# Kernel optimization log

Hardware: AMD Instinct MI355X
Metric: run time of the kernel (lower is better)

The kernel has to match this reference:

```python
import jax, jax.numpy as jnp
import numpy as np

START_INDEX = 3
STOP_INDEX = 4
NEG = -10000.0


def _lstm_dir(x, w_ih, w_hh, b_ih, b_hh, reverse):
    """Single-direction LSTM over [T, D] with batch=1, zero init state (torch default)."""
    H = w_hh.shape[1]
    xg = x @ w_ih.T + (b_ih + b_hh)  # [T, 4H] precomputed input contribution
    def step(carry, xg_t):
        h, c = carry
        g = xg_t + h @ w_hh.T          # [4H], torch gate order i,f,g,o
        i, f, gg, o = jnp.split(g, 4)
        c = jax.nn.sigmoid(f) * c + jax.nn.sigmoid(i) * jnp.tanh(gg)
        h = jax.nn.sigmoid(o) * jnp.tanh(c)
        return (h, c), h
    init = (jnp.zeros((H,), x.dtype), jnp.zeros((H,), x.dtype))
    _, hs = jax.lax.scan(step, init, xg, reverse=reverse)
    return hs  # [T, H], time-aligned for both directions


def _viterbi(feats, transitions):
    """Vectorized log-domain Viterbi DP; transitions[next, prev]."""
    L = transitions.shape[0]
    init = jnp.full((L,), NEG, feats.dtype).at[START_INDEX].set(0.0)
    def step(fv, feat):
        scores = fv[None, :] + transitions  # [L_next, L_prev]
        fv_new = jnp.max(scores, axis=1) + feat
        return fv_new, jnp.argmax(scores, axis=1)
    fv, bps = jax.lax.scan(step, init, feats)
    terminal = fv + transitions[STOP_INDEX]
    best = jnp.argmax(terminal)
    score = terminal[best]
    def back(lbl, bp):
        return bp[lbl], lbl
    _, path = jax.lax.scan(back, best, bps, reverse=True)  # path[t] = best label at t
    return score, path


def setup_inputs() -> dict:
    E, H, L, T = 512, 1024, 5, 8192
    key = jax.random.key(0)
    ks = jax.random.split(key, 24)
    s = 1.0 / np.sqrt(H)
    u = lambda k, shape: jax.random.uniform(k, shape, jnp.float32, -s, s)
    inp = {
        "hours": jax.random.normal(ks[0], (T, E), jnp.float32),
        # layer 0 forward / reverse
        "w_ih_l0": u(ks[1], (4 * H, E)), "w_hh_l0": u(ks[2], (4 * H, H)),
        "b_ih_l0": u(ks[3], (4 * H,)), "b_hh_l0": u(ks[4], (4 * H,)),
        "w_ih_l0r": u(ks[5], (4 * H, E)), "w_hh_l0r": u(ks[6], (4 * H, H)),
        "b_ih_l0r": u(ks[7], (4 * H,)), "b_hh_l0r": u(ks[8], (4 * H,)),
        # layer 1 forward / reverse (input is 2H)
        "w_ih_l1": u(ks[9], (4 * H, 2 * H)), "w_hh_l1": u(ks[10], (4 * H, H)),
        "b_ih_l1": u(ks[11], (4 * H,)), "b_hh_l1": u(ks[12], (4 * H,)),
        "w_ih_l1r": u(ks[13], (4 * H, 2 * H)), "w_hh_l1r": u(ks[14], (4 * H, H)),
        "b_ih_l1r": u(ks[15], (4 * H,)), "b_hh_l1r": u(ks[16], (4 * H,)),
        # hidden2label
        "w_out": u(ks[17], (L, 2 * H)), "b_out": u(ks[18], (L,)),
    }
    trans = jax.random.normal(ks[19], (L, L), jnp.float32)
    trans = trans.at[START_INDEX, :].set(NEG).at[:, STOP_INDEX].set(NEG)
    inp["transitions"] = trans
    return inp


def reference(hours, w_ih_l0, w_hh_l0, b_ih_l0, b_hh_l0,
              w_ih_l0r, w_hh_l0r, b_ih_l0r, b_hh_l0r,
              w_ih_l1, w_hh_l1, b_ih_l1, b_hh_l1,
              w_ih_l1r, w_hh_l1r, b_ih_l1r, b_hh_l1r,
              w_out, b_out, transitions):
    # layer 0 bidirectional
    h0f = _lstm_dir(hours, w_ih_l0, w_hh_l0, b_ih_l0, b_hh_l0, reverse=False)
    h0b = _lstm_dir(hours, w_ih_l0r, w_hh_l0r, b_ih_l0r, b_hh_l0r, reverse=True)
    h0 = jnp.concatenate([h0f, h0b], axis=-1)  # [T, 2H]
    # layer 1 bidirectional
    h1f = _lstm_dir(h0, w_ih_l1, w_hh_l1, b_ih_l1, b_hh_l1, reverse=False)
    h1b = _lstm_dir(h0, w_ih_l1r, w_hh_l1r, b_ih_l1r, b_hh_l1r, reverse=True)
    h1 = jnp.concatenate([h1f, h1b], axis=-1)  # [T, 2H]
    feats = h1 @ w_out.T + b_out               # [T, L]
    score, path = _viterbi(feats, transitions)
    return score, path
```

## Files before the change

kernel.cpp:

```cpp
#include <hip/hip_runtime.h>
#include <hip/hip_bf16.h>
#include <stdint.h>

#define T_SEQ 8192
#define E_IN  512
#define H_DIM 1024
#define FH    4096
#define H2    2048
#define NLAB  5
#define NEGV  (-10000.0f)

typedef __attribute__((ext_vector_type(8))) short bf16x8;
typedef __attribute__((ext_vector_type(4))) float f32x4;

__device__ __forceinline__ uint32_t f2bf(float f) {
  uint32_t x = __float_as_uint(f);
  return (x + 0x7FFFu + ((x >> 16) & 1u)) >> 16;
}
__device__ __forceinline__ uint32_t pack2bf(float lo, float hi) {
  return f2bf(lo) | (f2bf(hi) << 16);
}
__device__ __forceinline__ float bf2f(uint32_t b) {
  return __uint_as_float(b << 16);
}
__device__ __forceinline__ float fsig(float x) { return 1.0f / (1.0f + __expf(-x)); }
__device__ __forceinline__ float ftanh(float x) {
  float ax = fabsf(x);
  float e = __expf(-2.0f * ax);
  float t = (1.0f - e) / (1.0f + e);
  return copysignf(t, x);
}

__global__ void bias_kernel(const float* bi0, const float* bh0,
                            const float* bi0r, const float* bh0r,
                            const float* bi1, const float* bh1,
                            const float* bi1r, const float* bh1r,
                            float* bsum) {
  int i = blockIdx.x * blockDim.x + threadIdx.x;
  int d = i >> 12, j = i & 4095;
  const float *a, *b;
  switch (d) {
    case 0:  a = bi0;  b = bh0;  break;
    case 1:  a = bi0r; b = bh0r; break;
    case 2:  a = bi1;  b = bh1;  break;
    default: a = bi1r; b = bh1r; break;
  }
  bsum[i] = a[j] + b[j];
}

template <bool AF32>
__global__ __launch_bounds__(256) void gemm_xg(const void* Aptr, const float* Bt,
                                               const float* bias, uint16_t* C, int K) {
  const int m0 = blockIdx.x * 128;
  const int n0 = blockIdx.y * 128;
  __shared__ uint32_t As[128 * 20];
  __shared__ uint32_t Bs[128 * 20];
  const int tid  = threadIdx.x;
  const int lane = tid & 63;
  const int wave = tid >> 6;
  const int wr = wave >> 1, wc = wave & 1;
  const int row = tid >> 1;
  const int seg = tid & 1;

  f32x4 acc[4][4];
#pragma unroll
  for (int i = 0; i < 4; ++i)
#pragma unroll
    for (int j = 0; j < 4; ++j)
      acc[i][j] = (f32x4){0.0f, 0.0f, 0.0f, 0.0f};

  const int nk = K / 32;
  for (int kk = 0; kk < nk; ++kk) {
    const int k0 = kk * 32;
    uint32_t* dst = &As[row * 20 + seg * 8];
    if (AF32) {
      const float4* src = (const float4*)((const float*)Aptr + (size_t)(m0 + row) * K + k0 + seg * 16);
      uint32_t w[8];
#pragma unroll
      for (int u = 0; u < 4; ++u) {
        float4 v = src[u];
        w[2 * u]     = pack2bf(v.x, v.y);
        w[2 * u + 1] = pack2bf(v.z, v.w);
      }
      ((uint4*)dst)[0] = make_uint4(w[0], w[1], w[2], w[3]);
      ((uint4*)dst)[1] = make_uint4(w[4], w[5], w[6], w[7]);
    } else {
      const uint4* src = (const uint4*)((const uint16_t*)Aptr + (size_t)(m0 + row) * K + k0 + seg * 16);
      ((uint4*)dst)[0] = src[0];
      ((uint4*)dst)[1] = src[1];
    }
    {
      const float4* src = (const float4*)(Bt + (size_t)(n0 + row) * K + k0 + seg * 16);
      uint32_t w[8];
#pragma unroll
      for (int u = 0; u < 4; ++u) {
        float4 v = src[u];
        w[2 * u]     = pack2bf(v.x, v.y);
        w[2 * u + 1] = pack2bf(v.z, v.w);
      }
      uint32_t* dstb = &Bs[row * 20 + seg * 8];
      ((uint4*)dstb)[0] = make_uint4(w[0], w[1], w[2], w[3]);
      ((uint4*)dstb)[1] = make_uint4(w[4], w[5], w[6], w[7]);
    }
    __syncthreads();

    const int mfrag = lane & 15, kq = lane >> 4;
    bf16x8 af[4], bfr[4];
#pragma unroll
    for (int i = 0; i < 4; ++i) {
      af[i]  = *(const bf16x8*)&As[(wr * 64 + i * 16 + mfrag) * 20 + kq * 4];
      bfr[i] = *(const bf16x8*)&Bs[(wc * 64 + i * 16 + mfrag) * 20 + kq * 4];
    }
#pragma unroll
    for (int i = 0; i < 4; ++i)
#pragma unroll
      for (int j = 0; j < 4; ++j)
        acc[i][j] = __builtin_amdgcn_mfma_f32_16x16x32_bf16(af[i], bfr[j], acc[i][j], 0, 0, 0);
    __syncthreads();
  }

  const int colq = lane & 15, rowq = lane >> 4;
#pragma unroll
  for (int j = 0; j < 4; ++j) {
    const int col = n0 + wc * 64 + j * 16 + colq;
    const float bv = bias[col];
    const int pcol = ((col & 1023) >> 4) * 64 + (col >> 10) * 16 + (col & 15);
#pragma unroll
    for (int i = 0; i < 4; ++i) {
#pragma unroll
      for (int r = 0; r < 4; ++r) {
        const int rrow = m0 + wr * 64 + i * 16 + rowq * 4 + r;
        C[(size_t)rrow * FH + pcol] = (uint16_t)f2bf(acc[i][j][r] + bv);
      }
    }
  }
}

__global__ __launch_bounds__(512, 2) void lstm_layer(
    const float* __restrict__ whh_f, const float* __restrict__ whh_b,
    const uint16_t* __restrict__ xg_f, const uint16_t* __restrict__ xg_b,
    uint32_t* hpub_f, uint32_t* hpub_b, uint16_t* __restrict__ hseq) {
  const int bid = blockIdx.x;
  const int dir = bid & 1;
  const int g   = bid >> 1;
  const int hb  = g * 16;
  const int tid = threadIdx.x;
  const int jj  = tid & 15;
  const int kc  = tid >> 4;
  const int lane = tid & 63;
  const int wv   = tid >> 6;

  const float*    whh  = dir ? whh_b : whh_f;
  const uint16_t* xg   = dir ? xg_b : xg_f;
  uint32_t*       hpub = dir ? hpub_b : hpub_f;
  const int colbase    = dir ? H_DIM : 0;

  __shared__ __align__(16) float h_lds[H_DIM];
  __shared__ __align__(16) float part2[8][16][4];

  float Wr[4][32];
#pragma unroll
  for (int q = 0; q < 4; ++q) {
    const float4* wrow = (const float4*)(whh + (size_t)(q * H_DIM + hb + jj) * H_DIM + kc * 32);
#pragma unroll
    for (int i4 = 0; i4 < 8; ++i4) {
      float4 v = wrow[i4];
      Wr[q][i4 * 4 + 0] = v.x; Wr[q][i4 * 4 + 1] = v.y;
      Wr[q][i4 * 4 + 2] = v.z; Wr[q][i4 * 4 + 3] = v.w;
    }
  }

  float cstate = 0.0f;

  for (int s = 0; s < T_SEQ; ++s) {
    const int t = dir ? (T_SEQ - 1 - s) : s;

    float xgv = 0.0f;
    if (tid < 64) xgv = bf2f(xg[(size_t)t * FH + g * 64 + tid]);

    if (s == 0) {
      ((float2*)h_lds)[tid] = make_float2(0.f, 0.f);
    } else {
      const uint64_t etag = ((uint64_t)(uint32_t)((s - 1) << 16) << 32) |
                            (uint32_t)((s - 1) << 16);
      unsigned long long* hp =
          (unsigned long long*)(hpub + (((s - 1) & 1) ? H_DIM : 0)) + tid;
      unsigned long long v;
      for (;;) {
        v = __hip_atomic_load(hp, __ATOMIC_RELAXED, __HIP_MEMORY_SCOPE_AGENT);
        if ((((unsigned long long)v ^ etag) & 0xFFFF0000FFFF0000ull) == 0) break;
      }
      h_lds[2 * tid]     = bf2f((uint32_t)v & 0xFFFFu);
      h_lds[2 * tid + 1] = bf2f((uint32_t)(v >> 32) & 0xFFFFu);
    }
    __syncthreads();

    float a0 = 0.f, a1 = 0.f, a2 = 0.f, a3 = 0.f;
#pragma unroll
    for (int ii = 0; ii < 8; ++ii) {
      float4 h4 = ((const float4*)h_lds)[kc * 8 + ii];
      a0 += Wr[0][ii * 4 + 0] * h4.x; a0 += Wr[0][ii * 4 + 1] * h4.y;
      a0 += Wr[0][ii * 4 + 2] * h4.z; a0 += Wr[0][ii * 4 + 3] * h4.w;
      a1 += Wr[1][ii * 4 + 0] * h4.x; a1 += Wr[1][ii * 4 + 1] * h4.y;
      a1 += Wr[1][ii * 4 + 2] * h4.z; a1 += Wr[1][ii * 4 + 3] * h4.w;
      a2 += Wr[2][ii * 4 + 0] * h4.x; a2 += Wr[2][ii * 4 + 1] * h4.y;
      a2 += Wr[2][ii * 4 + 2] * h4.z; a2 += Wr[2][ii * 4 + 3] * h4.w;
      a3 += Wr[3][ii * 4 + 0] * h4.x; a3 += Wr[3][ii * 4 + 1] * h4.y;
      a3 += Wr[3][ii * 4 + 2] * h4.z; a3 += Wr[3][ii * 4 + 3] * h4.w;
    }
    a0 += __shfl_xor(a0, 16); a1 += __shfl_xor(a1, 16);
    a2 += __shfl_xor(a2, 16); a3 += __shfl_xor(a3, 16);
    a0 += __shfl_xor(a0, 32); a1 += __shfl_xor(a1, 32);
    a2 += __shfl_xor(a2, 32); a3 += __shfl_xor(a3, 32);
    if (lane < 16)
      *(float4*)&part2[wv][lane][0] = make_float4(a0, a1, a2, a3);
    __syncthreads();

    if (tid < 64) {
      const int gq = tid >> 4, gjj = tid & 15;
      float gval = part2[0][gjj][gq] + part2[1][gjj][gq] +
                   part2[2][gjj][gq] + part2[3][gjj][gq] +
                   part2[4][gjj][gq] + part2[5][gjj][gq] +
                   part2[6][gjj][gq] + part2[7][gjj][gq] + xgv;
      float gi = gval;
      float gf = __shfl(gval, gjj + 16);
      float gg = __shfl(gval, gjj + 32);
      float go = __shfl(gval, gjj + 48);
      if (gq == 0) {
        float i_s = fsig(gi), f_s = fsig(gf), g_t = ftanh(gg), o_s = fsig(go);
        cstate = f_s * cstate + i_s * g_t;
        float h = o_s * ftanh(cstate);
        uint32_t w = ((uint32_t)s << 16) | f2bf(h);
        __hip_atomic_store(&hpub[(s & 1) * H_DIM + hb + gjj], w,
                           __ATOMIC_RELAXED, __HIP_MEMORY_SCOPE_AGENT);
        hseq[(size_t)t * H2 + colbase + hb + gjj] = (uint16_t)(w & 0xFFFFu);
      }
    }
  }
}

__global__ __launch_bounds__(256) void feats_kernel(const uint16_t* __restrict__ h1,
                                                    const float* __restrict__ wout,
                                                    const float* __restrict__ bout,
                                                    float* __restrict__ feats) {
  const int lane = threadIdx.x & 63;
  const int wid  = (blockIdx.x * blockDim.x + threadIdx.x) >> 6;
  const int nwaves = (gridDim.x * blockDim.x) >> 6;

  float wreg[5][32];
#pragma unroll
  for (int j = 0; j < 5; ++j) {
    const float4* src = (const float4*)(wout + j * H2 + lane * 32);
#pragma unroll
    for (int u = 0; u < 8; ++u) {
      float4 v = src[u];
      wreg[j][u * 4 + 0] = v.x; wreg[j][u * 4 + 1] = v.y;
      wreg[j][u * 4 + 2] = v.z; wreg[j][u * 4 + 3] = v.w;
    }
  }
  for (int t = wid; t < T_SEQ; t += nwaves) {
    const uint32_t* hrow = (const uint32_t*)(h1 + (size_t)t * H2) + lane * 16;
    float acc[5] = {0.f, 0.f, 0.f, 0.f, 0.f};
#pragma unroll
    for (int u = 0; u < 16; ++u) {
      uint32_t w2 = hrow[u];
      float hlo = __uint_as_float(w2 << 16);
      float hhi = __uint_as_float(w2 & 0xFFFF0000u);
#pragma unroll
      for (int j = 0; j < 5; ++j)
        acc[j] += wreg[j][u * 2] * hlo + wreg[j][u * 2 + 1] * hhi;
    }
#pragma unroll
    for (int off = 32; off >= 1; off >>= 1)
#pragma unroll
      for (int j = 0; j < 5; ++j)
        acc[j] += __shfl_xor(acc[j], off);
    if (lane < 5) feats[t * NLAB + lane] = acc[lane] + bout[lane];
  }
}

__global__ __launch_bounds__(256) void viterbi_kernel(const float* __restrict__ feats,
                                                      const float* __restrict__ trans,
                                                      float* __restrict__ out) {
  __shared__ float scanM[256][26];
  __shared__ uint16_t bpsL[T_SEQ];
  __shared__ int bestL;
  const int tid = threadIdx.x;

  float tr[5][5];
#pragma unroll
  for (int n = 0; n < 5; ++n)
#pragma unroll
    for (int p = 0; p < 5; ++p) tr[n][p] = trans[n * 5 + p];

  float C[5][5];
  {
    const int t0 = tid * 32;
    const float* f = feats + (size_t)t0 * 5;
#pragma unroll
    for (int n = 0; n < 5; ++n)
#pragma unroll
      for (int p = 0; p < 5; ++p) C[n][p] = tr[n][p] + f[n];
    for (int t = 1; t < 32; ++t) {
      const float* ft = feats + (size_t)(t0 + t) * 5;
      float Nw[5][5];
#pragma unroll
      for (int n = 0; n < 5; ++n) {
#pragma unroll
        for (int p = 0; p < 5; ++p) {
          float m = tr[n][0] + C[0][p];
#pragma unroll
          for (int k = 1; k < 5; ++k) m = fmaxf(m, tr[n][k] + C[k][p]);
          Nw[n][p] = m + ft[n];
        }
      }
#pragma unroll
      for (int n = 0; n < 5; ++n)
#pragma unroll
        for (int p = 0; p < 5; ++p) C[n][p] = Nw[n][p];
    }
#pragma unroll
    for (int n = 0; n < 5; ++n)
#pragma unroll
      for (int p = 0; p < 5; ++p) scanM[tid][n * 5 + p] = C[n][p];
  }
  __syncthreads();

  for (int d = 1; d < 256; d <<= 1) {
    float A[5][5], B[5][5];
    const bool has = (tid >= d);
#pragma unroll
    for (int n = 0; n < 5; ++n)
#pragma unroll
      for (int p = 0; p < 5; ++p) A[n][p] = scanM[tid][n * 5 + p];
    if (has) {
#pragma unroll
      for (int n = 0; n < 5; ++n)
#pragma unroll
        for (int p = 0; p < 5; ++p) B[n][p] = scanM[tid - d][n * 5 + p];
    }
    __syncthreads();
    if (has) {
#pragma unroll
      for (int n = 0; n < 5; ++n) {
#pragma unroll
        for (int p = 0; p < 5; ++p) {
          float m = A[n][0] + B[0][p];
#pragma unroll
          for (int k = 1; k < 5; ++k) m = fmaxf(m, A[n][k] + B[k][p]);
          scanM[tid][n * 5 + p] = m;
        }
      }
    }
    __syncthreads();
  }

  float fv[5];
  if (tid == 0) {
#pragma unroll
    for (int n = 0; n < 5; ++n) fv[n] = (n == 3) ? 0.0f : NEGV;
  } else {
#pragma unroll
    for (int n = 0; n < 5; ++n) {
      float m = scanM[tid - 1][n * 5 + 3];
#pragma unroll
      for (int p = 0; p < 5; ++p)
        if (p != 3) m = fmaxf(m, scanM[tid - 1][n * 5 + p] + NEGV);
      fv[n] = m;
    }
  }

  {
    const int t0 = tid * 32;
    for (int t = 0; t < 32; ++t) {
      const float* ft = feats + (size_t)(t0 + t) * 5;
      float nf[5];
      uint32_t bits = 0;
#pragma unroll
      for (int n = 0; n < 5; ++n) {
        float m = tr[n][0] + fv[0];
        int arg = 0;
#pragma unroll
        for (int p = 1; p < 5; ++p) {
          float s2 = tr[n][p] + fv[p];
          if (s2 > m) { m = s2; arg = p; }
        }
        nf[n] = m + ft[n];
        bits |= (uint32_t)arg << (3 * n);
      }
      bpsL[t0 + t] = (uint16_t)bits;
#pragma unroll
      for (int n = 0; n < 5; ++n) fv[n] = nf[n];
    }
    if (tid == 255) {
      float m = fv[0] + tr[4][0];
      int arg = 0;
#pragma unroll
      for (int p = 1; p < 5; ++p) {
        float s2 = fv[p] + tr[4][p];
        if (s2 > m) { m = s2; arg = p; }
      }
      out[0] = m;
      bestL = arg;
    }
  }
  __syncthreads();

  for (int d = 1; d < T_SEQ; d <<= 1) {
    uint32_t own[32], par[32];
#pragma unroll
    for (int k = 0; k < 32; ++k) {
      int t = tid + k * 256;
      own[k] = bpsL[t];
      par[k] = (t + d < T_SEQ) ? (uint32_t)bpsL[t + d] : 0u;
    }
    __syncthreads();
#pragma unroll
    for (int k = 0; k < 32; ++k) {
      int t = tid + k * 256;
      if (t + d < T_SEQ) {
        uint32_t fmp = own[k], gmp = par[k], r = 0;
#pragma unroll
        for (int x = 0; x < 5; ++x) {
          uint32_t j = (gmp >> (3 * x)) & 7u;
          uint32_t v = (fmp >> (3 * j)) & 7u;
          r |= v << (3 * x);
        }
        bpsL[t] = (uint16_t)r;
      }
    }
    __syncthreads();
  }

  const int best = bestL;
  for (int k = 0; k < 32; ++k) {
    int t = tid + k * 256;
    int lbl = (t == T_SEQ - 1) ? best : (int)((bpsL[t + 1] >> (3 * best)) & 7u);
    out[1 + t] = (float)lbl;
  }
}

extern "C" void kernel_launch(void* const* d_in, const int* in_sizes, int n_in,
                              void* d_out, int out_size, void* d_ws, size_t ws_size,
                              hipStream_t stream) {
  const float* hours     = (const float*)d_in[0];
  const float* w_ih_l0   = (const float*)d_in[1];
  const float* w_hh_l0   = (const float*)d_in[2];
  const float* b_ih_l0   = (const float*)d_in[3];
  const float* b_hh_l0   = (const float*)d_in[4];
  const float* w_ih_l0r  = (const float*)d_in[5];
  const float* w_hh_l0r  = (const float*)d_in[6];
  const float* b_ih_l0r  = (const float*)d_in[7];
  const float* b_hh_l0r  = (const float*)d_in[8];
  const float* w_ih_l1   = (const float*)d_in[9];
  const float* w_hh_l1   = (const float*)d_in[10];
  const float* b_ih_l1   = (const float*)d_in[11];
  const float* b_hh_l1   = (const float*)d_in[12];
  const float* w_ih_l1r  = (const float*)d_in[13];
  const float* w_hh_l1r  = (const float*)d_in[14];
  const float* b_ih_l1r  = (const float*)d_in[15];
  const float* b_hh_l1r  = (const float*)d_in[16];
  const float* w_out     = (const float*)d_in[17];
  const float* b_out     = (const float*)d_in[18];
  const float* transitions = (const float*)d_in[19];
  float* out = (float*)d_out;

  char* ws = (char*)d_ws;
  size_t off = 0;
  auto alloc = [&](size_t bytes) -> void* {
    void* p = ws + off;
    off += (bytes + 255) & ~(size_t)255;
    return p;
  };
  uint16_t* xgf   = (uint16_t*)alloc((size_t)T_SEQ * FH * 2);
  uint16_t* xgb   = (uint16_t*)alloc((size_t)T_SEQ * FH * 2);
  uint16_t* h0seq = (uint16_t*)alloc((size_t)T_SEQ * H2 * 2);
  uint16_t* h1seq = h0seq;
  float*    bsum  = (float*)alloc((size_t)4 * FH * 4);
  uint32_t* hpub  = (uint32_t*)alloc((size_t)2 * 2 * 2 * H_DIM * 4);
  float*    feats = (float*)alloc((size_t)T_SEQ * NLAB * 4);
  (void)ws_size; (void)in_sizes; (void)n_in; (void)out_size;

  bias_kernel<<<64, 256, 0, stream>>>(b_ih_l0, b_hh_l0, b_ih_l0r, b_hh_l0r,
                                      b_ih_l1, b_hh_l1, b_ih_l1r, b_hh_l1r, bsum);
  dim3 gg(64, 32);
  gemm_xg<true><<<gg, 256, 0, stream>>>(hours, w_ih_l0,  bsum + 0 * FH, xgf, E_IN);
  gemm_xg<true><<<gg, 256, 0, stream>>>(hours, w_ih_l0r, bsum + 1 * FH, xgb, E_IN);
  lstm_layer<<<128, 512, 0, stream>>>(w_hh_l0, w_hh_l0r, xgf, xgb,
                                      hpub + 0, hpub + 2048, h0seq);
  gemm_xg<false><<<gg, 256, 0, stream>>>(h0seq, w_ih_l1,  bsum + 2 * FH, xgf, H2);
  gemm_xg<false><<<gg, 256, 0, stream>>>(h0seq, w_ih_l1r, bsum + 3 * FH, xgb, H2);
  lstm_layer<<<128, 512, 0, stream>>>(w_hh_l1, w_hh_l1r, xgf, xgb,
                                      hpub + 4096, hpub + 6144, h1seq);
  feats_kernel<<<128, 256, 0, stream>>>(h1seq, w_out, b_out, feats);
  viterbi_kernel<<<1, 256, 0, stream>>>(feats, transitions, out);
}
```

Baseline: 32.38 ms.

## Assign two hidden units per wave in LSTM recurrence, drop second block barrier

```diff
diff --git a/kernel.cpp b/kernel.cpp
--- a/kernel.cpp
+++ b/kernel.cpp
@@ -145,10 +145,10 @@
   const int g   = bid >> 1;
   const int hb  = g * 16;
   const int tid = threadIdx.x;
-  const int jj  = tid & 15;
-  const int kc  = tid >> 4;
   const int lane = tid & 63;
   const int wv   = tid >> 6;
+  const int j0   = hb + 2 * wv;
+  const int ph   = lane >> 5;
 
   const float*    whh  = dir ? whh_b : whh_f;
   const uint16_t* xg   = dir ? xg_b : xg_f;
@@ -156,85 +156,77 @@
   const int colbase    = dir ? H_DIM : 0;
 
   __shared__ __align__(16) float h_lds[H_DIM];
-  __shared__ __align__(16) float part2[8][16][4];
-
-  float Wr[4][32];
-#pragma unroll
-  for (int q = 0; q < 4; ++q) {
-    const float4* wrow = (const float4*)(whh + (size_t)(q * H_DIM + hb + jj) * H_DIM + kc * 32);
-#pragma unroll
-    for (int i4 = 0; i4 < 8; ++i4) {
-      float4 v = wrow[i4];
-      Wr[q][i4 * 4 + 0] = v.x; Wr[q][i4 * 4 + 1] = v.y;
-      Wr[q][i4 * 4 + 2] = v.z; Wr[q][i4 * 4 + 3] = v.w;
-    }
-  }
+  __shared__ __align__(8)  float xg_lds[64];
+
+  float Wr[8][16];
+#pragma unroll
+  for (int q = 0; q < 4; ++q)
+#pragma unroll
+    for (int p = 0; p < 2; ++p) {
+      const float* row = whh + (size_t)(q * H_DIM + j0 + p) * H_DIM + lane;
+#pragma unroll
+      for (int i = 0; i < 16; ++i)
+        Wr[q * 2 + p][i] = row[i * 64];
+    }
 
   float cstate = 0.0f;
 
   for (int s = 0; s < T_SEQ; ++s) {
     const int t = dir ? (T_SEQ - 1 - s) : s;
 
-    float xgv = 0.0f;
-    if (tid < 64) xgv = bf2f(xg[(size_t)t * FH + g * 64 + tid]);
+    if (tid < 64) xg_lds[tid] = bf2f(xg[(size_t)t * FH + g * 64 + tid]);
 
     if (s == 0) {
       ((float2*)h_lds)[tid] = make_float2(0.f, 0.f);
     } else {
-      const uint64_t etag = ((uint64_t)(uint32_t)((s - 1) << 16) << 32) |
-                            (uint32_t)((s - 1) << 16);
+      const uint32_t et = (uint32_t)(s - 1) << 16;
+      const uint64_t etag = ((uint64_t)et << 32) | et;
       unsigned long long* hp =
           (unsigned long long*)(hpub + (((s - 1) & 1) ? H_DIM : 0)) + tid;
+      unsigned long long a = __hip_atomic_load(hp, __ATOMIC_RELAXED, __HIP_MEMORY_SCOPE_AGENT);
+      unsigned long long b = __hip_atomic_load(hp, __ATOMIC_RELAXED, __HIP_MEMORY_SCOPE_AGENT);
       unsigned long long v;
       for (;;) {
-        v = __hip_atomic_load(hp, __ATOMIC_RELAXED, __HIP_MEMORY_SCOPE_AGENT);
-        if ((((unsigned long long)v ^ etag) & 0xFFFF0000FFFF0000ull) == 0) break;
+        if (((a ^ etag) & 0xFFFF0000FFFF0000ull) == 0) { v = a; break; }
+        a = __hip_atomic_load(hp, __ATOMIC_RELAXED, __HIP_MEMORY_SCOPE_AGENT);
+        if (((b ^ etag) & 0xFFFF0000FFFF0000ull) == 0) { v = b; break; }
+        b = __hip_atomic_load(hp, __ATOMIC_RELAXED, __HIP_MEMORY_SCOPE_AGENT);
       }
       h_lds[2 * tid]     = bf2f((uint32_t)v & 0xFFFFu);
       h_lds[2 * tid + 1] = bf2f((uint32_t)(v >> 32) & 0xFFFFu);
     }
     __syncthreads();
 
-    float a0 = 0.f, a1 = 0.f, a2 = 0.f, a3 = 0.f;
-#pragma unroll
-    for (int ii = 0; ii < 8; ++ii) {
-      float4 h4 = ((const float4*)h_lds)[kc * 8 + ii];
-      a0 += Wr[0][ii * 4 + 0] * h4.x; a0 += Wr[0][ii * 4 + 1] * h4.y;
-      a0 += Wr[0][ii * 4 + 2] * h4.z; a0 += Wr[0][ii * 4 + 3] * h4.w;
-      a1 += Wr[1][ii * 4 + 0] * h4.x; a1 += Wr[1][ii * 4 + 1] * h4.y;
-      a1 += Wr[1][ii * 4 + 2] * h4.z; a1 += Wr[1][ii * 4 + 3] * h4.w;
-      a2 += Wr[2][ii * 4 + 0] * h4.x; a2 += Wr[2][ii * 4 + 1] * h4.y;
-      a2 += Wr[2][ii * 4 + 2] * h4.z; a2 += Wr[2][ii * 4 + 3] * h4.w;
-      a3 += Wr[3][ii * 4 + 0] * h4.x; a3 += Wr[3][ii * 4 + 1] * h4.y;
-      a3 += Wr[3][ii * 4 + 2] * h4.z; a3 += Wr[3][ii * 4 + 3] * h4.w;
-    }
-    a0 += __shfl_xor(a0, 16); a1 += __shfl_xor(a1, 16);
-    a2 += __shfl_xor(a2, 16); a3 += __shfl_xor(a3, 16);
-    a0 += __shfl_xor(a0, 32); a1 += __shfl_xor(a1, 32);
-    a2 += __shfl_xor(a2, 32); a3 += __shfl_xor(a3, 32);
-    if (lane < 16)
-      *(float4*)&part2[wv][lane][0] = make_float4(a0, a1, a2, a3);
-    __syncthreads();
-
-    if (tid < 64) {
-      const int gq = tid >> 4, gjj = tid & 15;
-      float gval = part2[0][gjj][gq] + part2[1][gjj][gq] +
-                   part2[2][gjj][gq] + part2[3][gjj][gq] +
-                   part2[4][gjj][gq] + part2[5][gjj][gq] +
-                   part2[6][gjj][gq] + part2[7][gjj][gq] + xgv;
-      float gi = gval;
-      float gf = __shfl(gval, gjj + 16);
-      float gg = __shfl(gval, gjj + 32);
-      float go = __shfl(gval, gjj + 48);
-      if (gq == 0) {
-        float i_s = fsig(gi), f_s = fsig(gf), g_t = ftanh(gg), o_s = fsig(go);
-        cstate = f_s * cstate + i_s * g_t;
-        float h = o_s * ftanh(cstate);
-        uint32_t w = ((uint32_t)s << 16) | f2bf(h);
-        __hip_atomic_store(&hpub[(s & 1) * H_DIM + hb + gjj], w,
-                           __ATOMIC_RELAXED, __HIP_MEMORY_SCOPE_AGENT);
-        hseq[(size_t)t * H2 + colbase + hb + gjj] = (uint16_t)(w & 0xFFFFu);
-      }
+    float acc[8] = {0.f, 0.f, 0.f, 0.f, 0.f, 0.f, 0.f, 0.f};
+#pragma unroll
+    for (int i = 0; i < 16; ++i) {
+      float hv = h_lds[i * 64 + lane];
+#pragma unroll
+      for (int vv = 0; vv < 8; ++vv) acc[vv] += Wr[vv][i] * hv;
+    }
+#pragma unroll
+    for (int off = 1; off <= 16; off <<= 1)
+#pragma unroll
+      for (int vv = 0; vv < 8; ++vv) acc[vv] += __shfl_xor(acc[vv], off);
+    float gv[4];
+#pragma unroll
+    for (int q = 0; q < 4; ++q) {
+      float mine = ph ? acc[q * 2 + 1] : acc[q * 2 + 0];
+      float send = ph ? acc[q * 2 + 0] : acc[q * 2 + 1];
+      gv[q] = mine + __shfl_xor(send, 32) + xg_lds[q * 16 + 2 * wv + ph];
+    }
+
+    float i_s = fsig(gv[0]), f_s = fsig(gv[1]), g_t = ftanh(gv[2]), o_s = fsig(gv[3]);
+    cstate = f_s * cstate + i_s * g_t;
+    float h = o_s * ftanh(cstate);
+    uint32_t myw = ((uint32_t)s << 16) | f2bf(h);
+    uint32_t otw = __shfl_xor(myw, 32);
+    if (lane == 0) {
+      unsigned long long pw = ((unsigned long long)otw << 32) | myw;
+      __hip_atomic_store((unsigned long long*)(hpub + (s & 1) * H_DIM + j0), pw,
+                         __ATOMIC_RELAXED, __HIP_MEMORY_SCOPE_AGENT);
+      ((uint32_t*)hseq)[((size_t)t * H2 + colbase + j0) >> 1] =
+          (myw & 0xFFFFu) | (otw << 16);
     }
   }
 }
```

New measurement: 60.98 ms. 1.88x slower.
